# Performance work log

Measured on AMD Instinct MI355X. Metric: run time of the kernel, lower is better.

Reference implementation:

```python
import jax
jax.config.update("jax_enable_x64", True)  # codes use *1e12 factors; need int64
import jax.numpy as jnp
import numpy as np

# HashRectsPt hyperparameters (module buffers)
W0, H0 = 512.0, 512.0
ALPHA = 1.2
GAMMA = 0.6
BX, BY = 0.5, 0.5
N_RECTS = 8192


def setup_inputs() -> dict:
    key = jax.random.key(0)
    k1, k2, k3 = jax.random.split(key, 3)
    xy = jax.random.uniform(k1, (N_RECTS, 2), minval=0.0, maxval=2000.0)
    wh = jax.random.uniform(k2, (N_RECTS, 2), minval=8.0, maxval=512.0)
    rects = jnp.concatenate([xy, wh], axis=1).astype(jnp.float32)  # [N,4] x,y,w,h
    conf = jax.random.uniform(k3, (N_RECTS,), dtype=jnp.float32)
    return {"rects": rects, "conf": conf}


def _hash_codes(rects):
    # HashRectsPt.__call__ -> packed single int64 code per rect
    x, y, w, h = rects[:, 0], rects[:, 1], rects[:, 2], rects[:, 3]
    log_alpha = jnp.log(jnp.float32(ALPHA))
    i = jnp.round((jnp.log(jnp.float32(W0)) - jnp.log(w)) / log_alpha)
    j = jnp.round((jnp.log(jnp.float32(H0)) - jnp.log(h)) / log_alpha)
    gamma_ratio = (1.0 - GAMMA) / (1.0 + GAMMA)
    di = (W0 * gamma_ratio) / (ALPHA ** i)
    dj = (H0 * gamma_ratio) / (ALPHA ** j)
    # b_is_relative=True branch
    qx = jnp.round(x / di - BX)
    qy = jnp.round(y / dj - BY)
    codes = (qx.astype(jnp.int64)
             + qy.astype(jnp.int64) * 10_000
             + i.astype(jnp.int64) * 100_000_000
             + j.astype(jnp.int64) * 1_000_000_000_000)
    return codes  # [N] int64


def reference(rects, conf):
    codes = _hash_codes(rects)                         # [N]
    n = codes.shape[0]
    # torch.unique with data-dependent U -> padded fixed-size unique (U<=N);
    # pad value can never equal a real code, so padded columns match nothing.
    uniq = jnp.unique(codes, size=n, fill_value=jnp.iinfo(jnp.int64).min)  # [N]
    assign = codes[:, None] == uniq[None, :]           # [N, U] bool
    scores = conf[:, None] * assign.astype(conf.dtype)  # [N, U]
    # torch .max(dim=0) returns first max index; jnp.argmax matches.
    argidx = jnp.argmax(scores, axis=0)                # [U]
    return argidx
```

## Files before the change

kernel.cpp:

```cpp
#include <hip/hip_runtime.h>
#include <math.h>

#define N 8192
#define K1_TPB 256
#define K1_IB  32
#define K1_JS  16
#define K1_SL  (N / K1_JS)
#define K2_TPB 256

__device__ __forceinline__ unsigned pack_code_tab(float x, float y, float w, float h,
                                                  const float* __restrict__ s_pow) {
    const float LOG_ALPHA = (float)log((double)1.2f);
    const float LOGW0     = (float)log(512.0);
    float i_f = rintf((LOGW0 - (float)log((double)w)) / LOG_ALPHA);
    float j_f = rintf((LOGW0 - (float)log((double)h)) / LOG_ALPHA);
    int ii = (int)i_f, jj = (int)j_f;
    float qx = rintf(x / (128.0f / s_pow[ii]) - 0.5f);
    float qy = rintf(y / (128.0f / s_pow[jj]) - 0.5f);
    return ((unsigned)jj << 27) | ((unsigned)ii << 22)
         | ((unsigned)(int)qy << 11) | (unsigned)(int)qx;
}

__global__ void __launch_bounds__(K1_TPB)
k_flags(const float4* __restrict__ rects, const float* __restrict__ conf,
        unsigned* __restrict__ code32, unsigned char* __restrict__ flag16,
        int* __restrict__ out) {
    __shared__ unsigned long long s_w[K1_SL];
    __shared__ float s_pow[24];
    const int t  = threadIdx.x;
    const int ib = blockIdx.x, js = blockIdx.y;
    const int jb = js * K1_SL;
    const int i  = ib * K1_TPB + t;

    if (t < 24) s_pow[t] = (float)pow((double)1.2f, (double)t);
    __syncthreads();

    float4 ri = rects[i];
    unsigned ci = pack_code_tab(ri.x, ri.y, ri.z, ri.w, s_pow);
    unsigned long long wi = ((unsigned long long)ci << 32)
                          | (unsigned long long)__float_as_uint(conf[i]);
    if (js == 0) { code32[i] = ci; out[i] = 0; }

    #pragma unroll
    for (int c = 0; c < 2; ++c) {
        int j = jb + t + c * K1_TPB;
        float4 rj = rects[j];
        unsigned cj = pack_code_tab(rj.x, rj.y, rj.z, rj.w, s_pow);
        s_w[t + c * K1_TPB] = ((unsigned long long)cj << 32)
                            | (unsigned long long)__float_as_uint(conf[j]);
    }
    __syncthreads();

    bool lose = false;
    #pragma unroll 8
    for (int k = 0; k < K1_SL; ++k) {
        unsigned long long wj = s_w[k];
        bool ceq = (unsigned)(wj >> 32) == ci;
        bool g   = wj > wi;
        bool e   = wj == wi;
        bool d   = (jb + k) < i;
        lose = lose | (ceq & (g | (e & d)));
    }
    flag16[i * K1_JS + js] = lose ? 1 : 0;
}

__global__ void __launch_bounds__(K2_TPB)
k_rank(const unsigned* __restrict__ code32, const uint4* __restrict__ flag16v,
       const float* __restrict__ conf, int* __restrict__ out) {
    __shared__ unsigned s_v[N];
    __shared__ int s_r[K2_TPB];
    const int t = threadIdx.x, b = blockIdx.x;

    #pragma unroll 4
    for (int c = 0; c < N / K2_TPB; ++c) {
        int j = t + c * K2_TPB;
        uint4 f = flag16v[j];
        unsigned lose = f.x | f.y | f.z | f.w;
        unsigned code = code32[j];
        s_v[j] = lose ? 0xFFFFFFFFu : code;
    }
    __syncthreads();

    const int il = t & 31, seg = t >> 5;
    const int i = b * 32 + il;
    unsigned ci = s_v[i];
    const uint4* sv4 = (const uint4*)&s_v[seg * 1024];
    int r = 0;
    #pragma unroll 8
    for (int k = 0; k < 256; ++k) {
        uint4 v = sv4[k];
        r += (int)(v.x < ci) + (int)(v.y < ci) + (int)(v.z < ci) + (int)(v.w < ci);
    }
    s_r[seg * 32 + il] = r;
    __syncthreads();

    if (t < 32) {
        int gi = b * 32 + t;
        int rr = 0;
        #pragma unroll
        for (int s = 0; s < 8; ++s) rr += s_r[s * 32 + t];
        if (s_v[gi] != 0xFFFFFFFFu) {
            out[rr] = (conf[gi] == 0.0f) ? 0 : gi;
        }
    }
}

extern "C" void kernel_launch(void* const* d_in, const int* in_sizes, int n_in,
                              void* d_out, int out_size, void* d_ws, size_t ws_size,
                              hipStream_t stream) {
    const float4* rects = (const float4*)d_in[0];
    const float*  conf  = (const float*)d_in[1];
    int* out = (int*)d_out;

    char* ws = (char*)d_ws;
    unsigned*      code32 = (unsigned*)ws;
    unsigned char* flag16 = (unsigned char*)(ws + N * 4);

    k_flags<<<dim3(K1_IB, K1_JS), K1_TPB, 0, stream>>>(rects, conf, code32, flag16, out);
    k_rank <<<dim3(N / 32),       K2_TPB, 0, stream>>>(code32, (const uint4*)flag16, conf, out);
}
```

Baseline: 88.01 us.

## Register-block four rows per thread in flag kernel and simplify loser compare

The pairwise loser-flag kernel now has each thread handle four query rects against a 256-entry shared slice, so each shared-memory load is reused across four comparisons. The equal-code-and-larger test becomes a single 64-bit range check against a precomputed upper bound, and shared memory is read as 128-bit pairs. The grid changes to 8x32 blocks and the flag rows widen to 32 bytes, so the rank kernel now reads two uint4 per element. This cuts shared-memory traffic per comparison but raises register use and lowers block count, which could reduce occupancy.

Result: slower. 112.3 us (+27.5%).

```diff
diff --git a/kernel.cpp b/kernel.cpp
--- a/kernel.cpp
+++ b/kernel.cpp
@@ -2,11 +2,12 @@
 #include <math.h>
 
 #define N 8192
-#define K1_TPB 256
-#define K1_IB  32
-#define K1_JS  16
-#define K1_SL  (N / K1_JS)
-#define K2_TPB 256
+#define F_TPB 256
+#define F_IT  4
+#define F_IB  8
+#define F_JS  32
+#define F_SL  256
+#define R_TPB 256
 
 __device__ __forceinline__ unsigned pack_code_tab(float x, float y, float w, float h,
                                                   const float* __restrict__ s_pow) {
@@ -21,63 +22,71 @@
          | ((unsigned)(int)qy << 11) | (unsigned)(int)qx;
 }
 
-__global__ void __launch_bounds__(K1_TPB)
+__global__ void __launch_bounds__(F_TPB)
 k_flags(const float4* __restrict__ rects, const float* __restrict__ conf,
-        unsigned* __restrict__ code32, unsigned char* __restrict__ flag16,
+        unsigned* __restrict__ code32, unsigned char* __restrict__ flagrow,
         int* __restrict__ out) {
-    __shared__ unsigned long long s_w[K1_SL];
+    __shared__ unsigned long long s_w[F_SL];
     __shared__ float s_pow[24];
-    const int t  = threadIdx.x;
-    const int ib = blockIdx.x, js = blockIdx.y;
-    const int jb = js * K1_SL;
-    const int i  = ib * K1_TPB + t;
+    const int t = threadIdx.x, ib = blockIdx.x, js = blockIdx.y;
+    const int jb = js * F_SL;
 
     if (t < 24) s_pow[t] = (float)pow((double)1.2f, (double)t);
     __syncthreads();
 
-    float4 ri = rects[i];
-    unsigned ci = pack_code_tab(ri.x, ri.y, ri.z, ri.w, s_pow);
-    unsigned long long wi = ((unsigned long long)ci << 32)
-                          | (unsigned long long)__float_as_uint(conf[i]);
-    if (js == 0) { code32[i] = ci; out[i] = 0; }
-
+    {
+        float4 rj = rects[jb + t];
+        unsigned cj = pack_code_tab(rj.x, rj.y, rj.z, rj.w, s_pow);
+        s_w[t] = ((unsigned long long)cj << 32)
+               | (unsigned long long)__float_as_uint(conf[jb + t]);
+    }
+    unsigned long long wi[F_IT], bd[F_IT];
+    int ii[F_IT];
     #pragma unroll
-    for (int c = 0; c < 2; ++c) {
-        int j = jb + t + c * K1_TPB;
-        float4 rj = rects[j];
-        unsigned cj = pack_code_tab(rj.x, rj.y, rj.z, rj.w, s_pow);
-        s_w[t + c * K1_TPB] = ((unsigned long long)cj << 32)
-                            | (unsigned long long)__float_as_uint(conf[j]);
+    for (int m = 0; m < F_IT; ++m) {
+        int i = ib * (F_TPB * F_IT) + m * F_TPB + t;
+        ii[m] = i;
+        float4 ri = rects[i];
+        unsigned ci = pack_code_tab(ri.x, ri.y, ri.z, ri.w, s_pow);
+        wi[m] = ((unsigned long long)ci << 32)
+              | (unsigned long long)__float_as_uint(conf[i]);
+        bd[m] = (wi[m] | 0xFFFFFFFFULL) + 1ULL;
+        if (js == 0) { code32[i] = ci; out[i] = 0; }
     }
     __syncthreads();
 
-    bool lose = false;
-    #pragma unroll 8
-    for (int k = 0; k < K1_SL; ++k) {
-        unsigned long long wj = s_w[k];
-        bool ceq = (unsigned)(wj >> 32) == ci;
-        bool g   = wj > wi;
-        bool e   = wj == wi;
-        bool d   = (jb + k) < i;
-        lose = lose | (ceq & (g | (e & d)));
+    int l[F_IT] = {0, 0, 0, 0};
+    const ulonglong2* s2 = (const ulonglong2*)s_w;
+    #pragma unroll 4
+    for (int k = 0; k < F_SL / 2; ++k) {
+        ulonglong2 wj = s2[k];
+        int jg0 = jb + 2 * k, jg1 = jg0 + 1;
+        #pragma unroll
+        for (int m = 0; m < F_IT; ++m) {
+            l[m] |= (int)(((wj.x > wi[m]) & (wj.x < bd[m])) |
+                          ((wj.x == wi[m]) & (jg0 < ii[m])));
+            l[m] |= (int)(((wj.y > wi[m]) & (wj.y < bd[m])) |
+                          ((wj.y == wi[m]) & (jg1 < ii[m])));
+        }
     }
-    flag16[i * K1_JS + js] = lose ? 1 : 0;
+    #pragma unroll
+    for (int m = 0; m < F_IT; ++m)
+        flagrow[ii[m] * F_JS + js] = (unsigned char)l[m];
 }
 
-__global__ void __launch_bounds__(K2_TPB)
-k_rank(const unsigned* __restrict__ code32, const uint4* __restrict__ flag16v,
+__global__ void __launch_bounds__(R_TPB)
+k_rank(const unsigned* __restrict__ code32, const uint4* __restrict__ flagv,
        const float* __restrict__ conf, int* __restrict__ out) {
     __shared__ unsigned s_v[N];
-    __shared__ int s_r[K2_TPB];
+    __shared__ int s_r[R_TPB];
     const int t = threadIdx.x, b = blockIdx.x;
 
     #pragma unroll 4
-    for (int c = 0; c < N / K2_TPB; ++c) {
-        int j = t + c * K2_TPB;
-        uint4 f = flag16v[j];
-        unsigned lose = f.x | f.y | f.z | f.w;
-        unsigned code = code32[j];
-        s_v[j] = lose ? 0xFFFFFFFFu : code;
+    for (int c = 0; c < N / R_TPB; ++c) {
+        int j = t + c * R_TPB;
+        uint4 f0 = flagv[2 * j], f1 = flagv[2 * j + 1];
+        unsigned lose = f0.x | f0.y | f0.z | f0.w | f1.x | f1.y | f1.z | f1.w;
+        s_v[j] = lose ? 0xFFFFFFFFu : code32[j];
     }
     __syncthreads();
 
@@ -113,9 +122,9 @@
     int* out = (int*)d_out;
 
     char* ws = (char*)d_ws;
-    unsigned*      code32 = (unsigned*)ws;
-    unsigned char* flag16 = (unsigned char*)(ws + N * 4);
+    unsigned*      code32  = (unsigned*)ws;
+    unsigned char* flagrow = (unsigned char*)(ws + N * 4);
 
-    k_flags<<<dim3(K1_IB, K1_JS), K1_TPB, 0, stream>>>(rects, conf, code32, flag16, out);
-    k_rank <<<dim3(N / 32),       K2_TPB, 0, stream>>>(code32, (const uint4*)flag16, conf, out);
+    k_flags<<<dim3(F_IB, F_JS), F_TPB, 0, stream>>>(rects, conf, code32, flagrow, out);
+    k_rank <<<dim3(N / 32),     R_TPB, 0, stream>>>(code32, (const uint4*)flagrow, conf, out);
 }
```
